# Kernel optimization log

Hardware: AMD Instinct MI355X
Metric: run time of the kernel (lower is better)

Reference implementation:

```python
import jax, jax.numpy as jnp
import numpy as np

POS_DIM = 60  # position_embed_dim


def sincos_pos_embed(pos, dim):
    # pos: [..., 3] -> [..., dim]; dim//3 channels per coordinate, half sin / half cos
    d = dim // 3            # 20
    half = d // 2           # 10
    omega = 1.0 / (10000.0 ** (jnp.arange(half, dtype=pos.dtype) / half))
    out = pos[..., None] * omega                     # [..., 3, half]
    emb = jnp.concatenate([jnp.sin(out), jnp.cos(out)], axis=-1)  # [..., 3, d]
    return emb.reshape(pos.shape[:-1] + (3 * d,))


def setup_inputs() -> dict:
    key = jax.random.key(0)
    ks = jax.random.split(key, 20)
    B, N, K = 2, 16384, 24
    d_points, d_model = 64, 128
    s = 0.02
    inp = {
        "features": jax.random.normal(ks[0], (B, N, d_points), jnp.float32),
        "xyz": jax.random.normal(ks[1], (B, N, 3), jnp.float32),
        "knn_idx": jax.random.randint(ks[2], (B, N, K), 0, N),
        "knn_xyz": jax.random.normal(ks[3], (B, N, K, 3), jnp.float32),
        "fc1_w": jax.random.normal(ks[4], (d_points, d_model), jnp.float32) * s,
        "fc1_b": jnp.zeros((d_model,), jnp.float32),
        "fc2_w": jax.random.normal(ks[5], (d_model, d_model), jnp.float32) * s,
        "fc2_b": jnp.zeros((d_model,), jnp.float32),
        "d1_w": jax.random.normal(ks[6], (POS_DIM, d_model), jnp.float32) * s,
        "d1_b": jnp.zeros((d_model,), jnp.float32),
        "d2_w": jax.random.normal(ks[7], (d_model, d_model), jnp.float32) * s,
        "d2_b": jnp.zeros((d_model,), jnp.float32),
        "g1_w": jax.random.normal(ks[8], (d_model, d_model), jnp.float32) * s,
        "g1_b": jnp.zeros((d_model,), jnp.float32),
        "g2_w": jax.random.normal(ks[9], (d_model, d_model), jnp.float32) * s,
        "g2_b": jnp.zeros((d_model,), jnp.float32),
    }
    return inp


def reference(features, xyz, knn_idx, knn_xyz,
              fc1_w, fc1_b, fc2_w, fc2_b,
              d1_w, d1_b, d2_w, d2_b,
              g1_w, g1_b, g2_w, g2_b):
    B = features.shape[0]
    x = features @ fc1_w + fc1_b                       # [B,N,D]
    # index_points: gather neighbor features (q=x, k=v=gathered)
    kv = x[jnp.arange(B)[:, None, None], knn_idx]      # [B,N,K,D]
    g_xyz = xyz[:, :, None] - knn_xyz                  # [B,N,K,3]
    g_emb = sincos_pos_embed(g_xyz, POS_DIM)           # [B,N,K,60]
    pos_enc = jax.nn.relu(g_emb @ d1_w + d1_b) @ d2_w + d2_b   # [B,N,K,D]
    h = x[:, :, None] - kv + pos_enc                   # [B,N,K,D]
    attn = jax.nn.relu(h @ g1_w + g1_b) @ g2_w + g2_b  # [B,N,K,D]
    attn = jax.nn.softmax(attn / np.sqrt(kv.shape[-1]), axis=-2)  # softmax over K
    res = jnp.einsum('bmnf,bmnf->bmf', attn, kv + pos_enc)
    res = res @ fc2_w + fc2_b + x
    return res, attn
```

## Files before the change

### kernel.cpp

```cpp
#include <hip/hip_runtime.h>
#include <hip/hip_bf16.h>
#include <math.h>

constexpr int BB = 2;
constexpr int NN = 16384;
constexpr int KK = 24;
constexpr int DM = 128;
constexpr int DP = 64;

constexpr int PPB = 4;
constexpr int RR  = PPB * KK;

typedef __bf16 v8bf __attribute__((ext_vector_type(8)));
typedef float  v4f  __attribute__((ext_vector_type(4)));

constexpr int LDA128 = 136;
constexpr int LDA64  = 72;

constexpr int OFF_FC1T = 0;
constexpr int OFF_D1T  = 8192;
constexpr int OFF_D2T  = 16384;
constexpr int OFF_G1T  = 32768;
constexpr int OFF_G2T  = 49152;
constexpr int OFF_FC2T = 65536;
constexpr int W_TOTAL  = 81920;

__global__ __launch_bounds__(256) void prep_kernel(
    const float* __restrict__ fc1_w, const float* __restrict__ fc2_w,
    const float* __restrict__ d1_w,  const float* __restrict__ d2_w,
    const float* __restrict__ g1_w,  const float* __restrict__ g2_w,
    __hip_bfloat16* __restrict__ wbuf)
{
    const int i = blockIdx.x * 256 + threadIdx.x;
    if (i >= W_TOTAL) return;
    float v;
    if (i < OFF_D1T) {
        const int j = i, n = j >> 6, k = j & 63;
        v = fc1_w[k * DM + n];
    } else if (i < OFF_D2T) {
        const int j = i - OFF_D1T, n = j >> 6, k = j & 63;
        v = (k < 60) ? d1_w[k * DM + n] : 0.f;
    } else if (i < OFF_G1T) {
        const int j = i - OFF_D2T, n = j >> 7, k = j & 127;
        v = d2_w[k * DM + n];
    } else if (i < OFF_G2T) {
        const int j = i - OFF_G1T, n = j >> 7, k = j & 127;
        v = g1_w[k * DM + n];
    } else if (i < OFF_FC2T) {
        const int j = i - OFF_G2T, n = j >> 7, k = j & 127;
        v = g2_w[k * DM + n];
    } else {
        const int j = i - OFF_FC2T, f = j >> 7, g = j & 127;
        v = fc2_w[g * DM + f];
    }
    wbuf[i] = __float2bfloat16(v);
}

template <int MT, int NKT, int LDA, int LDB>
__device__ __forceinline__ void mm_frags(
    const __hip_bfloat16* As, const __hip_bfloat16* __restrict__ Bt,
    int c0, int lane, v4f (&acc)[MT][2])
{
    const int ln = lane & 15, quad = lane >> 4;
    #pragma unroll
    for (int mt = 0; mt < MT; ++mt) {
        acc[mt][0] = (v4f)0.f;
        acc[mt][1] = (v4f)0.f;
    }
    __builtin_amdgcn_s_setprio(1);
    #pragma unroll
    for (int kt = 0; kt < NKT; ++kt) {
        const int k0 = kt * 32 + quad * 8;
        const v8bf b0 = *(const v8bf*)(Bt + (c0 + ln) * LDB + k0);
        const v8bf b1 = *(const v8bf*)(Bt + (c0 + 16 + ln) * LDB + k0);
        #pragma unroll
        for (int mt = 0; mt < MT; ++mt) {
            const v8bf a = *(const v8bf*)(As + (mt * 16 + ln) * LDA + k0);
            acc[mt][0] = __builtin_amdgcn_mfma_f32_16x16x32_bf16(a, b0, acc[mt][0], 0, 0, 0);
            acc[mt][1] = __builtin_amdgcn_mfma_f32_16x16x32_bf16(a, b1, acc[mt][1], 0, 0, 0);
        }
    }
    __builtin_amdgcn_s_setprio(0);
}

__global__ __launch_bounds__(256) void fc1_kernel(
    const float* __restrict__ feat,
    const __hip_bfloat16* __restrict__ fc1t,
    const float* __restrict__ fc1_b,
    __hip_bfloat16* __restrict__ x_bf)
{
    __shared__ alignas(16) __hip_bfloat16 s_f[32 * LDA64];
    const int tid = threadIdx.x;
    const int r0  = blockIdx.x * 32;
    for (int e = tid; e < 32 * DP; e += 256) {
        const int r = e >> 6, k = e & 63;
        s_f[r * LDA64 + k] = __float2bfloat16(feat[(size_t)(r0 + r) * DP + k]);
    }
    __syncthreads();
    const int w = tid >> 6, lane = tid & 63;
    const int ln = lane & 15, quad = lane >> 4;
    const int c0 = w * 32;
    v4f acc[2][2];
    mm_frags<2, 2, LDA64, 64>(s_f, fc1t, c0, lane, acc);
    #pragma unroll
    for (int nl = 0; nl < 2; ++nl) {
        const int col = c0 + nl * 16 + ln;
        const float bb = fc1_b[col];
        #pragma unroll
        for (int mt = 0; mt < 2; ++mt)
            #pragma unroll
            for (int r = 0; r < 4; ++r) {
                const int row = mt * 16 + quad * 4 + r;
                x_bf[(size_t)(r0 + row) * DM + col] = __float2bfloat16(acc[mt][nl][r] + bb);
            }
    }
}

__device__ __forceinline__ int zoff(int row, int col) {
    const int h = (row + (row >> 3)) & 15;
    return (row << 7) + ((((col >> 3) ^ h) & 15) << 3) + (col & 7);
}

__device__ __forceinline__ unsigned pk2(float a, float b) {
    __hip_bfloat16 ha = __float2bfloat16(a), hb = __float2bfloat16(b);
    unsigned ua = *reinterpret_cast<unsigned short*>(&ha);
    unsigned ub = *reinterpret_cast<unsigned short*>(&hb);
    return ua | (ub << 16);
}
__device__ __forceinline__ float unlo(unsigned u) {
    unsigned v = u << 16; return *reinterpret_cast<float*>(&v);
}
__device__ __forceinline__ float unhi(unsigned u) {
    unsigned v = u & 0xffff0000u; return *reinterpret_cast<float*>(&v);
}

__global__ __launch_bounds__(256, 3) void fused_kernel(
    const __hip_bfloat16* __restrict__ x_bf,
    const float* __restrict__ xyz,
    const int*   __restrict__ knn_idx,
    const float* __restrict__ knn_xyz,
    const __hip_bfloat16* __restrict__ wbuf,
    const float* __restrict__ d1_b, const float* __restrict__ d2_b,
    const float* __restrict__ g1_b, const float* __restrict__ g2_b,
    const float* __restrict__ fc2_b,
    float* __restrict__ out_res,
    float* __restrict__ out_attn)
{
    __shared__ alignas(16) __hip_bfloat16 s_A[RR * LDA128];
    __shared__ alignas(16) __hip_bfloat16 s_Z[RR * DM];
    __shared__ alignas(16) __hip_bfloat16 s_xm[PPB * DM];

    __hip_bfloat16* s_ge = s_A;
    int* s_idx = reinterpret_cast<int*>(s_A + RR * LDA64);

    const int tid = threadIdx.x;
    const int pt0 = blockIdx.x * PPB;
    const int b   = pt0 >> 14;
    const int w = tid >> 6, lane = tid & 63;
    const int ln = lane & 15, quad = lane >> 4;
    const int c0 = w * 32;
    const bool lo = (quad < 2);

    if (tid < RR) s_idx[tid] = knn_idx[(size_t)pt0 * KK + tid];
    if (tid < PPB * DM / 8)
        *reinterpret_cast<v8bf*>(s_xm + tid * 8) =
            *(const v8bf*)(x_bf + (size_t)pt0 * DM + tid * 8);
    if (tid < RR)
        *reinterpret_cast<uint2*>(s_ge + tid * LDA64 + 60) = make_uint2(0u, 0u);
    for (int e = tid; e < RR * 30; e += 256) {
        const int row = e / 30;
        const int rem = e - row * 30;
        const int c = rem / 10;
        const int i = rem - c * 10;
        const int g = pt0 + row / 24;
        const float pv = xyz[(size_t)g * 3 + c] - knn_xyz[((size_t)pt0 * KK + row) * 3 + c];
        const float om = exp2f(-(float)i * 1.3287712379549449f);
        float sv, cv;
        __sincosf(pv * om, &sv, &cv);
        s_ge[row * LDA64 + c * 20 + i]      = __float2bfloat16(sv);
        s_ge[row * LDA64 + c * 20 + 10 + i] = __float2bfloat16(cv);
    }
    __syncthreads();

    v4f acc[6][2];

    v8bf gv[6];
    {
        const size_t xbase = (size_t)b * NN * DM;
        #pragma unroll
        for (int i = 0; i < 6; ++i) {
            const int e = tid + i * 256;
            const int row = e >> 4, part = e & 15;
            gv[i] = *(const v8bf*)(x_bf + xbase + (size_t)s_idx[row] * DM + part * 8);
        }
    }
    mm_frags<6, 2, LDA64, 64>(s_A, wbuf + OFF_D1T, c0, lane, acc);
    #pragma unroll
    for (int i = 0; i < 6; ++i) {
        const int e = tid + i * 256;
        const int row = e >> 4, part = e & 15;
        *reinterpret_cast<v8bf*>(&s_Z[zoff(row, part * 8)]) = gv[i];
    }
    __syncthreads();
    {
        const float bb0 = d1_b[c0 + ln], bb1 = d1_b[c0 + 16 + ln];
        #pragma unroll
        for (int mt = 0; mt < 6; ++mt) {
            const int row0 = mt * 16 + quad * 4;
            #pragma unroll
            for (int r = 0; r < 4; ++r) {
                s_A[(row0 + r) * LDA128 + c0 + ln]      = __float2bfloat16(fmaxf(acc[mt][0][r] + bb0, 0.f));
                s_A[(row0 + r) * LDA128 + c0 + 16 + ln] = __float2bfloat16(fmaxf(acc[mt][1][r] + bb1, 0.f));
            }
        }
    }
    __syncthreads();

    mm_frags<6, 4, LDA128, DM>(s_A, wbuf + OFF_D2T, c0, lane, acc);
    __syncthreads();
    unsigned kvpk[6][2][2];
    {
        const float bb0 = d2_b[c0 + ln], bb1 = d2_b[c0 + 16 + ln];
        #pragma unroll
        for (int mt = 0; mt < 6; ++mt) {
            constexpr int pl_[6] = {0,0,1,2,2,3};
            constexpr int ph_[6] = {0,1,1,2,3,3};
            const int row0 = mt * 16 + quad * 4;
            const int p = (pl_[mt] == ph_[mt]) ? pl_[mt] : (lo ? pl_[mt] : ph_[mt]);
            const float xm0 = __bfloat162float(s_xm[p * DM + c0 + ln]);
            const float xm1 = __bfloat162float(s_xm[p * DM + c0 + 16 + ln]);
            float kp0[4], kp1[4];
            #pragma unroll
            for (int r = 0; r < 4; ++r) {
                const int row = row0 + r;
                const float pe0 = acc[mt][0][r] + bb0;
                const float pe1 = acc[mt][1][r] + bb1;
                const float kv0 = __bfloat162float(s_Z[zoff(row, c0 + ln)]);
                const float kv1 = __bfloat162float(s_Z[zoff(row, c0 + 16 + ln)]);
                s_A[row * LDA128 + c0 + ln]      = __float2bfloat16(xm0 - kv0 + pe0);
                s_A[row * LDA128 + c0 + 16 + ln] = __float2bfloat16(xm1 - kv1 + pe1);
                kp0[r] = kv0 + pe0;
                kp1[r] = kv1 + pe1;
            }
            kvpk[mt][0][0] = pk2(kp0[0], kp0[1]);
            kvpk[mt][0][1] = pk2(kp0[2], kp0[3]);
            kvpk[mt][1][0] = pk2(kp1[0], kp1[1]);
            kvpk[mt][1][1] = pk2(kp1[2], kp1[3]);
        }
    }
    __syncthreads();

    mm_frags<6, 4, LDA128, DM>(s_A, wbuf + OFF_G1T, c0, lane, acc);
    __syncthreads();
    {
        const float bb0 = g1_b[c0 + ln], bb1 = g1_b[c0 + 16 + ln];
        #pragma unroll
        for (int mt = 0; mt < 6; ++mt) {
            const int row0 = mt * 16 + quad * 4;
            #pragma unroll
            for (int r = 0; r < 4; ++r) {
                s_A[(row0 + r) * LDA128 + c0 + ln]      = __float2bfloat16(fmaxf(acc[mt][0][r] + bb0, 0.f));
                s_A[(row0 + r) * LDA128 + c0 + 16 + ln] = __float2bfloat16(fmaxf(acc[mt][1][r] + bb1, 0.f));
            }
        }
    }
    __syncthreads();

    mm_frags<6, 4, LDA128, DM>(s_A, wbuf + OFF_G2T, c0, lane, acc);
    {
        const float C = 0.08838834764831845f * 1.4426950408889634f;
        const float sb0 = g2_b[c0 + ln] * C, sb1 = g2_b[c0 + 16 + ln] * C;
        #pragma unroll
        for (int mt = 0; mt < 6; ++mt)
            #pragma unroll
            for (int r = 0; r < 4; ++r) {
                acc[mt][0][r] = fmaf(acc[mt][0][r], C, sb0);
                acc[mt][1][r] = fmaf(acc[mt][1][r], C, sb1);
            }

        constexpr int pl_[6] = {0,0,1,2,2,3};
        constexpr int ph_[6] = {0,1,1,2,3,3};

        float mx[4][2];
        #pragma unroll
        for (int p = 0; p < 4; ++p) { mx[p][0] = -1e30f; mx[p][1] = -1e30f; }
        #pragma unroll
        for (int mt = 0; mt < 6; ++mt)
            #pragma unroll
            for (int nl = 0; nl < 2; ++nl) {
                const float m4 = fmaxf(fmaxf(acc[mt][nl][0], acc[mt][nl][1]),
                                       fmaxf(acc[mt][nl][2], acc[mt][nl][3]));
                if (pl_[mt] == ph_[mt]) {
                    mx[pl_[mt]][nl] = fmaxf(mx[pl_[mt]][nl], m4);
                } else {
                    mx[pl_[mt]][nl] = fmaxf(mx[pl_[mt]][nl], lo ? m4 : -1e30f);
                    mx[ph_[mt]][nl] = fmaxf(mx[ph_[mt]][nl], lo ? -1e30f : m4);
                }
            }
        #pragma unroll
        for (int p = 0; p < 4; ++p)
            #pragma unroll
            for (int nl = 0; nl < 2; ++nl) {
                float v = mx[p][nl];
                v = fmaxf(v, __shfl_xor(v, 16));
                v = fmaxf(v, __shfl_xor(v, 32));
                mx[p][nl] = v;
            }

        float sm[4][2];
        #pragma unroll
        for (int p = 0; p < 4; ++p) { sm[p][0] = 0.f; sm[p][1] = 0.f; }
        #pragma unroll
        for (int mt = 0; mt < 6; ++mt)
            #pragma unroll
            for (int nl = 0; nl < 2; ++nl) {
                const float mxv = (pl_[mt] == ph_[mt]) ? mx[pl_[mt]][nl]
                                  : (lo ? mx[pl_[mt]][nl] : mx[ph_[mt]][nl]);
                float es = 0.f;
                #pragma unroll
                for (int r = 0; r < 4; ++r) {
                    const float e = exp2f(acc[mt][nl][r] - mxv);
                    acc[mt][nl][r] = e;
                    es += e;
                }
                if (pl_[mt] == ph_[mt]) {
                    sm[pl_[mt]][nl] += es;
                } else {
                    sm[pl_[mt]][nl] += lo ? es : 0.f;
                    sm[ph_[mt]][nl] += lo ? 0.f : es;
                }
            }
        #pragma unroll
        for (int p = 0; p < 4; ++p)
            #pragma unroll
            for (int nl = 0; nl < 2; ++nl) {
                float v = sm[p][nl];
                v += __shfl_xor(v, 16);
                v += __shfl_xor(v, 32);
                sm[p][nl] = 1.f / v;
            }

        float rp[4][2];
        #pragma unroll
        for (int p = 0; p < 4; ++p) { rp[p][0] = 0.f; rp[p][1] = 0.f; }
        float* abase = out_attn + (size_t)pt0 * KK * DM;
        #pragma unroll
        for (int mt = 0; mt < 6; ++mt) {
            const int rowg0 = mt * 16 + quad * 4;
            #pragma unroll
            for (int nl = 0; nl < 2; ++nl) {
                const int col = c0 + nl * 16 + ln;
                const float invv = (pl_[mt] == ph_[mt]) ? sm[pl_[mt]][nl]
                                   : (lo ? sm[pl_[mt]][nl] : sm[ph_[mt]][nl]);
                const float kv0 = unlo(kvpk[mt][nl][0]);
                const float kv1 = unhi(kvpk[mt][nl][0]);
                const float kv2 = unlo(kvpk[mt][nl][1]);
                const float kv3 = unhi(kvpk[mt][nl][1]);
                const float a0 = acc[mt][nl][0] * invv;
                const float a1 = acc[mt][nl][1] * invv;
                const float a2 = acc[mt][nl][2] * invv;
                const float a3 = acc[mt][nl][3] * invv;
                abase[(size_t)(rowg0 + 0) * DM + col] = a0;
                abase[(size_t)(rowg0 + 1) * DM + col] = a1;
                abase[(size_t)(rowg0 + 2) * DM + col] = a2;
                abase[(size_t)(rowg0 + 3) * DM + col] = a3;
                const float ws = fmaf(a0, kv0, fmaf(a1, kv1, fmaf(a2, kv2, a3 * kv3)));
                if (pl_[mt] == ph_[mt]) {
                    rp[pl_[mt]][nl] += ws;
                } else {
                    rp[pl_[mt]][nl] += lo ? ws : 0.f;
                    rp[ph_[mt]][nl] += lo ? 0.f : ws;
                }
            }
        }
        #pragma unroll
        for (int p = 0; p < 4; ++p)
            #pragma unroll
            for (int nl = 0; nl < 2; ++nl) {
                float v = rp[p][nl];
                v += __shfl_xor(v, 16);
                v += __shfl_xor(v, 32);
                rp[p][nl] = v;
            }

        __syncthreads();
        if (quad == 0) {
            #pragma unroll
            for (int p = 0; p < 4; ++p) {
                s_A[p * LDA128 + c0 + ln]      = __float2bfloat16(rp[p][0]);
                s_A[p * LDA128 + c0 + 16 + ln] = __float2bfloat16(rp[p][1]);
            }
        }
    }
    __syncthreads();

    {
        v4f a2[1][2];
        mm_frags<1, 4, LDA128, DM>(s_A, wbuf + OFF_FC2T, c0, lane, a2);
        if (quad == 0) {
            #pragma unroll
            for (int nl = 0; nl < 2; ++nl) {
                const int col = c0 + nl * 16 + ln;
                const float bb = fc2_b[col];
                #pragma unroll
                for (int r = 0; r < 4; ++r)
                    out_res[(size_t)(pt0 + r) * DM + col] =
                        a2[0][nl][r] + bb + __bfloat162float(s_xm[r * DM + col]);
            }
        }
    }
}

extern "C" void kernel_launch(void* const* d_in, const int* in_sizes, int n_in,
                              void* d_out, int out_size, void* d_ws, size_t ws_size,
                              hipStream_t stream)
{
    const float* features = (const float*)d_in[0];
    const float* xyz      = (const float*)d_in[1];
    const int*   knn_idx  = (const int*)  d_in[2];
    const float* knn_xyz  = (const float*)d_in[3];
    const float* fc1_w    = (const float*)d_in[4];
    const float* fc1_b    = (const float*)d_in[5];
    const float* fc2_w    = (const float*)d_in[6];
    const float* fc2_b    = (const float*)d_in[7];
    const float* d1_w     = (const float*)d_in[8];
    const float* d1_b     = (const float*)d_in[9];
    const float* d2_w     = (const float*)d_in[10];
    const float* d2_b     = (const float*)d_in[11];
    const float* g1_w     = (const float*)d_in[12];
    const float* g1_b     = (const float*)d_in[13];
    const float* g2_w     = (const float*)d_in[14];
    const float* g2_b     = (const float*)d_in[15];

    __hip_bfloat16* x_bf = (__hip_bfloat16*)d_ws;
    __hip_bfloat16* wbuf = x_bf + (size_t)BB * NN * DM;
    float* out_res  = (float*)d_out;
    float* out_attn = out_res + (size_t)BB * NN * DM;

    prep_kernel<<<(W_TOTAL + 255) / 256, 256, 0, stream>>>(
        fc1_w, fc2_w, d1_w, d2_w, g1_w, g2_w, wbuf);
    fc1_kernel<<<(BB * NN) / 32, 256, 0, stream>>>(
        features, wbuf + OFF_FC1T, fc1_b, x_bf);
    fused_kernel<<<(BB * NN) / PPB, 256, 0, stream>>>(
        x_bf, xyz, knn_idx, knn_xyz, wbuf,
        d1_b, d2_b, g1_b, g2_b, fc2_b, out_res, out_attn);
}
```

Measured before the change: 670.5 us.

## Interleave MFMA output columns so each lane owns adjacent pairs, gather kv directly

Remaps the B-operand rows in the MFMA helper so each lane's two output tiles hold adjacent columns (2*ln, 2*ln+1). Bias loads, bf16 LDS stores, attention stores and the residual output can then use packed 32-bit or float2 accesses. The neighbour-feature gather now loads each lane's own column pair straight from global memory into registers, which removes the s_Z shared buffer and its swizzled staging. This lowers LDS use enough to raise occupancy to 4 blocks per SM. The price is narrower 4-byte scattered gathers in place of 16-byte vector loads, plus more registers held across the first matmul.

```diff
diff --git a/kernel.cpp b/kernel.cpp
--- a/kernel.cpp
+++ b/kernel.cpp
@@ -71,8 +71,8 @@
     #pragma unroll
     for (int kt = 0; kt < NKT; ++kt) {
         const int k0 = kt * 32 + quad * 8;
-        const v8bf b0 = *(const v8bf*)(Bt + (c0 + ln) * LDB + k0);
-        const v8bf b1 = *(const v8bf*)(Bt + (c0 + 16 + ln) * LDB + k0);
+        const v8bf b0 = *(const v8bf*)(Bt + (c0 + 2 * ln) * LDB + k0);
+        const v8bf b1 = *(const v8bf*)(Bt + (c0 + 2 * ln + 1) * LDB + k0);
         #pragma unroll
         for (int mt = 0; mt < MT; ++mt) {
             const v8bf a = *(const v8bf*)(As + (mt * 16 + ln) * LDA + k0);
@@ -81,6 +81,19 @@
         }
     }
     __builtin_amdgcn_s_setprio(0);
+}
+
+__device__ __forceinline__ unsigned pk2(float a, float b) {
+    __hip_bfloat16 ha = __float2bfloat16(a), hb = __float2bfloat16(b);
+    unsigned ua = *reinterpret_cast<unsigned short*>(&ha);
+    unsigned ub = *reinterpret_cast<unsigned short*>(&hb);
+    return ua | (ub << 16);
+}
+__device__ __forceinline__ float unlo(unsigned u) {
+    unsigned v = u << 16; return *reinterpret_cast<float*>(&v);
+}
+__device__ __forceinline__ float unhi(unsigned u) {
+    unsigned v = u & 0xffff0000u; return *reinterpret_cast<float*>(&v);
 }
 
 __global__ __launch_bounds__(256) void fc1_kernel(
@@ -102,39 +115,21 @@
     const int c0 = w * 32;
     v4f acc[2][2];
     mm_frags<2, 2, LDA64, 64>(s_f, fc1t, c0, lane, acc);
-    #pragma unroll
-    for (int nl = 0; nl < 2; ++nl) {
-        const int col = c0 + nl * 16 + ln;
-        const float bb = fc1_b[col];
+    {
+        const int col0 = c0 + 2 * ln;
+        const float2 bb = *(const float2*)(fc1_b + col0);
         #pragma unroll
         for (int mt = 0; mt < 2; ++mt)
             #pragma unroll
             for (int r = 0; r < 4; ++r) {
                 const int row = mt * 16 + quad * 4 + r;
-                x_bf[(size_t)(r0 + row) * DM + col] = __float2bfloat16(acc[mt][nl][r] + bb);
-            }
-    }
-}
-
-__device__ __forceinline__ int zoff(int row, int col) {
-    const int h = (row + (row >> 3)) & 15;
-    return (row << 7) + ((((col >> 3) ^ h) & 15) << 3) + (col & 7);
-}
-
-__device__ __forceinline__ unsigned pk2(float a, float b) {
-    __hip_bfloat16 ha = __float2bfloat16(a), hb = __float2bfloat16(b);
-    unsigned ua = *reinterpret_cast<unsigned short*>(&ha);
-    unsigned ub = *reinterpret_cast<unsigned short*>(&hb);
-    return ua | (ub << 16);
-}
-__device__ __forceinline__ float unlo(unsigned u) {
-    unsigned v = u << 16; return *reinterpret_cast<float*>(&v);
-}
-__device__ __forceinline__ float unhi(unsigned u) {
-    unsigned v = u & 0xffff0000u; return *reinterpret_cast<float*>(&v);
-}
-
-__global__ __launch_bounds__(256, 3) void fused_kernel(
+                *reinterpret_cast<unsigned*>(x_bf + (size_t)(r0 + row) * DM + col0) =
+                    pk2(acc[mt][0][r] + bb.x, acc[mt][1][r] + bb.y);
+            }
+    }
+}
+
+__global__ __launch_bounds__(256, 4) void fused_kernel(
     const __hip_bfloat16* __restrict__ x_bf,
     const float* __restrict__ xyz,
     const int*   __restrict__ knn_idx,
@@ -147,7 +142,6 @@
     float* __restrict__ out_attn)
 {
     __shared__ alignas(16) __hip_bfloat16 s_A[RR * LDA128];
-    __shared__ alignas(16) __hip_bfloat16 s_Z[RR * DM];
     __shared__ alignas(16) __hip_bfloat16 s_xm[PPB * DM];
 
     __hip_bfloat16* s_ge = s_A;
@@ -159,6 +153,7 @@
     const int w = tid >> 6, lane = tid & 63;
     const int ln = lane & 15, quad = lane >> 4;
     const int c0 = w * 32;
+    const int col0 = c0 + 2 * ln;
     const bool lo = (quad < 2);
 
     if (tid < RR) s_idx[tid] = knn_idx[(size_t)pt0 * KK + tid];
@@ -184,68 +179,55 @@
 
     v4f acc[6][2];
 
-    v8bf gv[6];
-    {
-        const size_t xbase = (size_t)b * NN * DM;
-        #pragma unroll
-        for (int i = 0; i < 6; ++i) {
-            const int e = tid + i * 256;
-            const int row = e >> 4, part = e & 15;
-            gv[i] = *(const v8bf*)(x_bf + xbase + (size_t)s_idx[row] * DM + part * 8);
+    unsigned kvg[6][4];
+    {
+        const __hip_bfloat16* xb = x_bf + (size_t)b * NN * DM + col0;
+        #pragma unroll
+        for (int mt = 0; mt < 6; ++mt) {
+            const int4 iv = *reinterpret_cast<const int4*>(&s_idx[mt * 16 + quad * 4]);
+            kvg[mt][0] = *(const unsigned*)(xb + (size_t)iv.x * DM);
+            kvg[mt][1] = *(const unsigned*)(xb + (size_t)iv.y * DM);
+            kvg[mt][2] = *(const unsigned*)(xb + (size_t)iv.z * DM);
+            kvg[mt][3] = *(const unsigned*)(xb + (size_t)iv.w * DM);
         }
     }
     mm_frags<6, 2, LDA64, 64>(s_A, wbuf + OFF_D1T, c0, lane, acc);
-    #pragma unroll
-    for (int i = 0; i < 6; ++i) {
-        const int e = tid + i * 256;
-        const int row = e >> 4, part = e & 15;
-        *reinterpret_cast<v8bf*>(&s_Z[zoff(row, part * 8)]) = gv[i];
-    }
-    __syncthreads();
-    {
-        const float bb0 = d1_b[c0 + ln], bb1 = d1_b[c0 + 16 + ln];
+    __syncthreads();
+    {
+        const float2 bb = *(const float2*)(d1_b + col0);
         #pragma unroll
         for (int mt = 0; mt < 6; ++mt) {
             const int row0 = mt * 16 + quad * 4;
             #pragma unroll
-            for (int r = 0; r < 4; ++r) {
-                s_A[(row0 + r) * LDA128 + c0 + ln]      = __float2bfloat16(fmaxf(acc[mt][0][r] + bb0, 0.f));
-                s_A[(row0 + r) * LDA128 + c0 + 16 + ln] = __float2bfloat16(fmaxf(acc[mt][1][r] + bb1, 0.f));
-            }
+            for (int r = 0; r < 4; ++r)
+                *reinterpret_cast<unsigned*>(&s_A[(row0 + r) * LDA128 + col0]) =
+                    pk2(fmaxf(acc[mt][0][r] + bb.x, 0.f), fmaxf(acc[mt][1][r] + bb.y, 0.f));
         }
     }
     __syncthreads();
 
     mm_frags<6, 4, LDA128, DM>(s_A, wbuf + OFF_D2T, c0, lane, acc);
     __syncthreads();
-    unsigned kvpk[6][2][2];
-    {
-        const float bb0 = d2_b[c0 + ln], bb1 = d2_b[c0 + 16 + ln];
+    {
+        const float2 bb = *(const float2*)(d2_b + col0);
+        constexpr int pl_[6] = {0,0,1,2,2,3};
+        constexpr int ph_[6] = {0,1,1,2,3,3};
         #pragma unroll
         for (int mt = 0; mt < 6; ++mt) {
-            constexpr int pl_[6] = {0,0,1,2,2,3};
-            constexpr int ph_[6] = {0,1,1,2,3,3};
             const int row0 = mt * 16 + quad * 4;
             const int p = (pl_[mt] == ph_[mt]) ? pl_[mt] : (lo ? pl_[mt] : ph_[mt]);
-            const float xm0 = __bfloat162float(s_xm[p * DM + c0 + ln]);
-            const float xm1 = __bfloat162float(s_xm[p * DM + c0 + 16 + ln]);
-            float kp0[4], kp1[4];
+            const unsigned xw = *reinterpret_cast<const unsigned*>(&s_xm[p * DM + col0]);
+            const float xm0 = unlo(xw), xm1 = unhi(xw);
             #pragma unroll
             for (int r = 0; r < 4; ++r) {
-                const int row = row0 + r;
-                const float pe0 = acc[mt][0][r] + bb0;
-                const float pe1 = acc[mt][1][r] + bb1;
-                const float kv0 = __bfloat162float(s_Z[zoff(row, c0 + ln)]);
-                const float kv1 = __bfloat162float(s_Z[zoff(row, c0 + 16 + ln)]);
-                s_A[row * LDA128 + c0 + ln]      = __float2bfloat16(xm0 - kv0 + pe0);
-                s_A[row * LDA128 + c0 + 16 + ln] = __float2bfloat16(xm1 - kv1 + pe1);
-                kp0[r] = kv0 + pe0;
-                kp1[r] = kv1 + pe1;
-            }
-            kvpk[mt][0][0] = pk2(kp0[0], kp0[1]);
-            kvpk[mt][0][1] = pk2(kp0[2], kp0[3]);
-            kvpk[mt][1][0] = pk2(kp1[0], kp1[1]);
-            kvpk[mt][1][1] = pk2(kp1[2], kp1[3]);
+                const float pe0 = acc[mt][0][r] + bb.x;
+                const float pe1 = acc[mt][1][r] + bb.y;
+                const float kv0 = unlo(kvg[mt][r]);
+                const float kv1 = unhi(kvg[mt][r]);
+                *reinterpret_cast<unsigned*>(&s_A[(row0 + r) * LDA128 + col0]) =
+                    pk2(xm0 - kv0 + pe0, xm1 - kv1 + pe1);
+                kvg[mt][r] = pk2(kv0 + pe0, kv1 + pe1);
+            }
         }
     }
     __syncthreads();
@@ -253,23 +235,24 @@
     mm_frags<6, 4, LDA128, DM>(s_A, wbuf + OFF_G1T, c0, lane, acc);
     __syncthreads();
     {
-        const float bb0 = g1_b[c0 + ln], bb1 = g1_b[c0 + 16 + ln];
+        const float2 bb = *(const float2*)(g1_b + col0);
         #pragma unroll
         for (int mt = 0; mt < 6; ++mt) {
             const int row0 = mt * 16 + quad * 4;
             #pragma unroll
-            for (int r = 0; r < 4; ++r) {
-                s_A[(row0 + r) * LDA128 + c0 + ln]      = __float2bfloat16(fmaxf(acc[mt][0][r] + bb0, 0.f));
-                s_A[(row0 + r) * LDA128 + c0 + 16 + ln] = __float2bfloat16(fmaxf(acc[mt][1][r] + bb1, 0.f));
-            }
+            for (int r = 0; r < 4; ++r)
+                *reinterpret_cast<unsigned*>(&s_A[(row0 + r) * LDA128 + col0]) =
+                    pk2(fmaxf(acc[mt][0][r] + bb.x, 0.f), fmaxf(acc[mt][1][r] + bb.y, 0.f));
         }
     }
     __syncthreads();
 
     mm_frags<6, 4, LDA128, DM>(s_A, wbuf + OFF_G2T, c0, lane, acc);
+    float rp[4][2];
     {
         const float C = 0.08838834764831845f * 1.4426950408889634f;
-        const float sb0 = g2_b[c0 + ln] * C, sb1 = g2_b[c0 + 16 + ln] * C;
+        const float2 gb = *(const float2*)(g2_b + col0);
+        const float sb0 = gb.x * C, sb1 = gb.y * C;
         #pragma unroll
         for (int mt = 0; mt < 6; ++mt)
             #pragma unroll
@@ -340,37 +323,31 @@
                 sm[p][nl] = 1.f / v;
             }
 
-        float rp[4][2];
         #pragma unroll
         for (int p = 0; p < 4; ++p) { rp[p][0] = 0.f; rp[p][1] = 0.f; }
-        float* abase = out_attn + (size_t)pt0 * KK * DM;
+        float* abase = out_attn + (size_t)pt0 * KK * DM + col0;
         #pragma unroll
         for (int mt = 0; mt < 6; ++mt) {
             const int rowg0 = mt * 16 + quad * 4;
-            #pragma unroll
-            for (int nl = 0; nl < 2; ++nl) {
-                const int col = c0 + nl * 16 + ln;
-                const float invv = (pl_[mt] == ph_[mt]) ? sm[pl_[mt]][nl]
-                                   : (lo ? sm[pl_[mt]][nl] : sm[ph_[mt]][nl]);
-                const float kv0 = unlo(kvpk[mt][nl][0]);
-                const float kv1 = unhi(kvpk[mt][nl][0]);
-                const float kv2 = unlo(kvpk[mt][nl][1]);
-                const float kv3 = unhi(kvpk[mt][nl][1]);
-                const float a0 = acc[mt][nl][0] * invv;
-                const float a1 = acc[mt][nl][1] * invv;
-                const float a2 = acc[mt][nl][2] * invv;
-                const float a3 = acc[mt][nl][3] * invv;
-                abase[(size_t)(rowg0 + 0) * DM + col] = a0;
-                abase[(size_t)(rowg0 + 1) * DM + col] = a1;
-                abase[(size_t)(rowg0 + 2) * DM + col] = a2;
-                abase[(size_t)(rowg0 + 3) * DM + col] = a3;
-                const float ws = fmaf(a0, kv0, fmaf(a1, kv1, fmaf(a2, kv2, a3 * kv3)));
-                if (pl_[mt] == ph_[mt]) {
-                    rp[pl_[mt]][nl] += ws;
-                } else {
-                    rp[pl_[mt]][nl] += lo ? ws : 0.f;
-                    rp[ph_[mt]][nl] += lo ? 0.f : ws;
-                }
+            const float inv0 = (pl_[mt] == ph_[mt]) ? sm[pl_[mt]][0]
+                               : (lo ? sm[pl_[mt]][0] : sm[ph_[mt]][0]);
+            const float inv1 = (pl_[mt] == ph_[mt]) ? sm[pl_[mt]][1]
+                               : (lo ? sm[pl_[mt]][1] : sm[ph_[mt]][1]);
+            float ws0 = 0.f, ws1 = 0.f;
+            #pragma unroll
+            for (int r = 0; r < 4; ++r) {
+                const float a0 = acc[mt][0][r] * inv0;
+                const float a1 = acc[mt][1][r] * inv1;
+                float2 st; st.x = a0; st.y = a1;
+                *reinterpret_cast<float2*>(abase + (size_t)(rowg0 + r) * DM) = st;
+                ws0 = fmaf(a0, unlo(kvg[mt][r]), ws0);
+                ws1 = fmaf(a1, unhi(kvg[mt][r]), ws1);
+            }
+            if (pl_[mt] == ph_[mt]) {
+                rp[pl_[mt]][0] += ws0; rp[pl_[mt]][1] += ws1;
+            } else {
+                rp[pl_[mt]][0] += lo ? ws0 : 0.f;  rp[pl_[mt]][1] += lo ? ws1 : 0.f;
+                rp[ph_[mt]][0] += lo ? 0.f : ws0;  rp[ph_[mt]][1] += lo ? 0.f : ws1;
             }
         }
         #pragma unroll
@@ -382,15 +359,13 @@
                 v += __shfl_xor(v, 32);
                 rp[p][nl] = v;
             }
-
-        __syncthreads();
-        if (quad == 0) {
-            #pragma unroll
-            for (int p = 0; p < 4; ++p) {
-                s_A[p * LDA128 + c0 + ln]      = __float2bfloat16(rp[p][0]);
-                s_A[p * LDA128 + c0 + 16 + ln] = __float2bfloat16(rp[p][1]);
-            }
-        }
+    }
+    __syncthreads();
+    if (quad == 0) {
+        #pragma unroll
+        for (int p = 0; p < 4; ++p)
+            *reinterpret_cast<unsigned*>(&s_A[p * LDA128 + col0]) =
+                pk2(rp[p][0], rp[p][1]);
     }
     __syncthreads();
 
@@ -398,14 +373,14 @@
         v4f a2[1][2];
         mm_frags<1, 4, LDA128, DM>(s_A, wbuf + OFF_FC2T, c0, lane, a2);
         if (quad == 0) {
-            #pragma unroll
-            for (int nl = 0; nl < 2; ++nl) {
-                const int col = c0 + nl * 16 + ln;
-                const float bb = fc2_b[col];
-                #pragma unroll
-                for (int r = 0; r < 4; ++r)
-                    out_res[(size_t)(pt0 + r) * DM + col] =
-                        a2[0][nl][r] + bb + __bfloat162float(s_xm[r * DM + col]);
+            const float2 bb = *(const float2*)(fc2_b + col0);
+            #pragma unroll
+            for (int r = 0; r < 4; ++r) {
+                const unsigned xw = *reinterpret_cast<const unsigned*>(&s_xm[r * DM + col0]);
+                float2 o;
+                o.x = a2[0][0][r] + bb.x + unlo(xw);
+                o.y = a2[0][1][r] + bb.y + unhi(xw);
+                *reinterpret_cast<float2*>(out_res + (size_t)(pt0 + r) * DM + col0) = o;
             }
         }
     }
```

After: 690.4 us. +3.0%, slower.
